# Kernel tuning notes

Hardware: AMD Instinct MI355X
Metric: run time of the kernel (lower is better)

Reference implementation:

```python
import jax, jax.numpy as jnp
import numpy as np

N, K = 4096, 256          # rays, samples per ray
V = 100000                # voxel table size
D = 64                    # field MLP hidden dim
SCALER = 7.0              # free-energy scaler from the source


def setup_inputs() -> dict:
    key = jax.random.key(0)
    ks = jax.random.split(key, 12)
    ray_start = jax.random.normal(ks[0], (N, 3), jnp.float32)
    rd = jax.random.normal(ks[1], (N, 3), jnp.float32)
    ray_dir = rd / jnp.linalg.norm(rd, axis=-1, keepdims=True)
    sampled_depth = jnp.sort(
        0.5 + 4.0 * jax.random.uniform(ks[2], (N, K), jnp.float32), axis=-1)
    sampled_dists = 0.02 * jax.random.uniform(ks[3], (N, K), jnp.float32)
    raw = jax.random.randint(ks[4], (N, K), 0, V + V // 4)
    sampled_idx = jnp.where(raw < V, raw, -1).astype(jnp.int64)
    voxel_color = 0.1 * jax.random.normal(ks[5], (V, 3), jnp.float32)
    W1 = jax.random.normal(ks[6], (6, D), jnp.float32) * (1.0 / np.sqrt(6.0))
    b1 = jnp.zeros((D,), jnp.float32)
    w_sigma = jax.random.normal(ks[7], (D, 1), jnp.float32) * (1.0 / np.sqrt(D))
    b_sigma = jnp.zeros((1,), jnp.float32)
    W_tex = jax.random.normal(ks[8], (D, 3), jnp.float32) * (1.0 / np.sqrt(D))
    b_tex = jnp.zeros((3,), jnp.float32)
    return dict(ray_start=ray_start, ray_dir=ray_dir,
                sampled_depth=sampled_depth, sampled_dists=sampled_dists,
                sampled_idx=sampled_idx, voxel_color=voxel_color,
                W1=W1, b1=b1, w_sigma=w_sigma, b_sigma=b_sigma,
                W_tex=W_tex, b_tex=b_tex)


def reference(ray_start, ray_dir, sampled_depth, sampled_dists, sampled_idx,
              voxel_color, W1, b1, w_sigma, b_sigma, W_tex, b_tex):
    mask = sampled_idx != -1                                   # [N,K] sample_mask
    # sampled_xyz = ray(start, dir, depth); sampled_dir broadcast of ray_dir
    xyz = ray_start[:, None, :] + ray_dir[:, None, :] * sampled_depth[..., None]
    dirs = jnp.broadcast_to(ray_dir[:, None, :], xyz.shape)    # [N,K,3]
    feat = jnp.concatenate([xyz, dirs], axis=-1)               # [N,K,6]
    # field_fn: small MLP -> sigma, texture
    h = jax.nn.relu(jnp.einsum('nkf,fd->nkd', feat, W1) + b1)  # [N,K,D]
    sigma = (jnp.einsum('nkd,do->nko', h, w_sigma) + b_sigma)[..., 0]  # [N,K]
    # voxel color embedding lookup (F.embedding); res=True adds it to texture
    idx_safe = jnp.where(mask, sampled_idx, 0)
    vcol = voxel_color[idx_safe]                               # [N,K,3] gather
    texture = jnp.einsum('nkd,dc->nkc', h, W_tex) + b_tex + vcol
    # free energy; masked_scatter == zero-out where mask is False
    free_energy = jnp.where(mask,
                            jax.nn.relu(sigma) * sampled_dists * SCALER, 0.0)
    texture = jnp.where(mask[..., None], texture, 0.0)
    # alpha compositing: a = 1-exp(-fe), b = exp(-cumsum(shifted fe))
    shifted = jnp.concatenate(
        [jnp.zeros((free_energy.shape[0], 1), free_energy.dtype),
         free_energy[:, :-1]], axis=-1)
    a = 1.0 - jnp.exp(-free_energy)
    b = jnp.exp(-jnp.cumsum(shifted, axis=-1))
    probs = a * b                                              # [N,K]
    depths = jnp.sum(sampled_depth * probs, axis=-1)           # [N]
    missed = 1.0 - jnp.sum(probs, axis=-1)                     # [N]
    colors = jnp.sum(texture * probs[..., None], axis=-2)      # [N,3]
    return colors, depths, missed, probs
```

## Files before the change

kernel.cpp:

```cpp
#include <hip/hip_runtime.h>

#define K_SAMP 256
#define D_HID 64
#define SCALER_FE 7.0f

typedef _Float16 half8  __attribute__((ext_vector_type(8)));
typedef __fp16   fp16x2 __attribute__((ext_vector_type(2)));
typedef float    f32x4  __attribute__((ext_vector_type(4)));

union H8U4 { half8 h; uint4 u; };
union H8P  { fp16x2 h2[4]; half8 h8; };

__device__ __forceinline__ half8 h8zero() {
    half8 a;
    #pragma unroll
    for (int j = 0; j < 8; ++j) a[j] = (_Float16)0.f;
    return a;
}

__global__ __launch_bounds__(256, 6)
void volrend_kernel(const float* __restrict__ ray_start,
                    const float* __restrict__ ray_dir,
                    const float* __restrict__ depth,
                    const float* __restrict__ dists,
                    const int*   __restrict__ vidx,
                    const float* __restrict__ vcol_tab,
                    const float* __restrict__ W1,
                    const float* __restrict__ b1,
                    const float* __restrict__ w_sigma,
                    const float* __restrict__ b_sigma,
                    const float* __restrict__ W_tex,
                    const float* __restrict__ b_tex,
                    float* __restrict__ out_colors,
                    float* __restrict__ out_depths,
                    float* __restrict__ out_missed,
                    float* __restrict__ out_probs) {
    __shared__ uint4 sFrag[6 * 64];
    __shared__ float sOut[K_SAMP][4];
    __shared__ float sTot[4];
    __shared__ float sRed[4][5];

    const int tid  = threadIdx.x;
    const int lane = tid & 63;
    const int wv   = tid >> 6;
    const int ray  = blockIdx.x;
    const int m    = lane & 15;
    const int g    = lane >> 4;

    if (tid < 64) {
        #pragma unroll
        for (int tt = 0; tt < 4; ++tt) {
            const int dim = 8 * (m >> 2) + (m & 3) + 4 * (tt & 1) + 32 * (tt >> 1);
            half8 a = h8zero();
            if (g == 0) {
                #pragma unroll
                for (int j = 0; j < 6; ++j) a[j] = (_Float16)W1[j * D_HID + dim];
                a[6] = (_Float16)b1[dim];
            }
            H8U4 c; c.h = a;
            sFrag[tt * 64 + lane] = c.u;
        }
        half8 a2a = h8zero(), a2b = h8zero();
        if (m < 4) {
            const int c = (m >= 1) ? (m - 1) : 0;
            #pragma unroll
            for (int j = 0; j < 8; ++j) {
                const int d = 8 * g + j;
                a2a[j] = (_Float16)((m == 0) ? w_sigma[d]      : W_tex[d * 3 + c]);
                a2b[j] = (_Float16)((m == 0) ? w_sigma[d + 32] : W_tex[(d + 32) * 3 + c]);
            }
        }
        H8U4 ca; ca.h = a2a; sFrag[4 * 64 + lane] = ca.u;
        H8U4 cb; cb.h = a2b; sFrag[5 * 64 + lane] = cb.u;
    }

    const float rs0 = ray_start[ray * 3 + 0];
    const float rs1 = ray_start[ray * 3 + 1];
    const float rs2 = ray_start[ray * 3 + 2];
    const float rd0 = ray_dir[ray * 3 + 0];
    const float rd1 = ray_dir[ray * 3 + 1];
    const float rd2 = ray_dir[ray * 3 + 2];
    const float bs  = b_sigma[0];
    const float bt0 = b_tex[0], bt1 = b_tex[1], bt2 = b_tex[2];

    __syncthreads();

    half8 a1[4];
    #pragma unroll
    for (int tt = 0; tt < 4; ++tt) { H8U4 c; c.u = sFrag[tt * 64 + lane]; a1[tt] = c.h; }
    H8U4 ca; ca.u = sFrag[4 * 64 + lane]; const half8 a2a = ca.h;
    H8U4 cb; cb.u = sFrag[5 * 64 + lane]; const half8 a2b = cb.h;

    f32x4 oinit = {0.f, 0.f, 0.f, 0.f};
    if (g == 0) { oinit[0] = bs; oinit[1] = bt0; oinit[2] = bt1; oinit[3] = bt2; }
    const f32x4 zero4 = {0.f, 0.f, 0.f, 0.f};

    const fp16x2 hc12 = __builtin_amdgcn_cvt_pkrtz(rd1, rd2);
    const fp16x2 hc3  = __builtin_amdgcn_cvt_pkrtz(1.0f, 0.0f);

    const size_t rayBase = (size_t)ray * K_SAMP;
    const int    qBase   = wv * 64;

    #pragma unroll
    for (int t = 0; t < 4; ++t) {
        const float dpt = depth[rayBase + qBase + 16 * t + m];
        const float fx = fmaf(rd0, dpt, rs0);
        const float fy = fmaf(rd1, dpt, rs1);
        const float fz = fmaf(rd2, dpt, rs2);
        H8P bb;
        bb.h2[0] = __builtin_amdgcn_cvt_pkrtz(fx, fy);
        bb.h2[1] = __builtin_amdgcn_cvt_pkrtz(fz, rd0);
        bb.h2[2] = hc12;
        bb.h2[3] = hc3;
        const f32x4 h0 = __builtin_amdgcn_mfma_f32_16x16x32_f16(a1[0], bb.h8, zero4, 0, 0, 0);
        const f32x4 h1 = __builtin_amdgcn_mfma_f32_16x16x32_f16(a1[1], bb.h8, zero4, 0, 0, 0);
        const f32x4 h2 = __builtin_amdgcn_mfma_f32_16x16x32_f16(a1[2], bb.h8, zero4, 0, 0, 0);
        const f32x4 h3 = __builtin_amdgcn_mfma_f32_16x16x32_f16(a1[3], bb.h8, zero4, 0, 0, 0);

        H8P p2a, p2b;
        p2a.h2[0] = __builtin_amdgcn_cvt_pkrtz(fmaxf(h0[0], 0.f), fmaxf(h0[1], 0.f));
        p2a.h2[1] = __builtin_amdgcn_cvt_pkrtz(fmaxf(h0[2], 0.f), fmaxf(h0[3], 0.f));
        p2a.h2[2] = __builtin_amdgcn_cvt_pkrtz(fmaxf(h1[0], 0.f), fmaxf(h1[1], 0.f));
        p2a.h2[3] = __builtin_amdgcn_cvt_pkrtz(fmaxf(h1[2], 0.f), fmaxf(h1[3], 0.f));
        p2b.h2[0] = __builtin_amdgcn_cvt_pkrtz(fmaxf(h2[0], 0.f), fmaxf(h2[1], 0.f));
        p2b.h2[1] = __builtin_amdgcn_cvt_pkrtz(fmaxf(h2[2], 0.f), fmaxf(h2[3], 0.f));
        p2b.h2[2] = __builtin_amdgcn_cvt_pkrtz(fmaxf(h3[0], 0.f), fmaxf(h3[1], 0.f));
        p2b.h2[3] = __builtin_amdgcn_cvt_pkrtz(fmaxf(h3[2], 0.f), fmaxf(h3[3], 0.f));

        f32x4 o = oinit;
        o = __builtin_amdgcn_mfma_f32_16x16x32_f16(a2a, p2a.h8, o, 0, 0, 0);
        o = __builtin_amdgcn_mfma_f32_16x16x32_f16(a2b, p2b.h8, o, 0, 0, 0);

        if (g == 0) {
            *(float4*)&sOut[qBase + 16 * t + m][0] = make_float4(o[0], o[1], o[2], o[3]);
        }
    }
    __syncthreads();

    const float dep = depth[rayBase + tid];
    const float dst = dists[rayBase + tid];
    const int   vi  = vidx[rayBase + tid];
    const bool  msk = (vi != -1);
    const int   vb  = (msk ? vi : 0) * 3;
    const float vc0 = vcol_tab[vb + 0];
    const float vc1 = vcol_tab[vb + 1];
    const float vc2 = vcol_tab[vb + 2];

    const float4 r4 = *(const float4*)&sOut[tid][0];
    float fe = 0.f, tA = 0.f, tB = 0.f, tC = 0.f;
    if (msk) {
        fe = fmaxf(r4.x, 0.f) * dst * SCALER_FE;
        tA = r4.y + vc0; tB = r4.z + vc1; tC = r4.w + vc2;
    }

    float x = fe;
    #pragma unroll
    for (int off = 1; off < 64; off <<= 1) {
        float v = __shfl_up(x, off, 64);
        if (lane >= off) x += v;
    }
    if (lane == 63) sTot[wv] = x;
    __syncthreads();
    float base = 0.f;
    #pragma unroll
    for (int w = 0; w < 3; ++w) {
        if (w < wv) base += sTot[w];
    }
    const float e0 = base + x - fe;
    const float p  = (1.0f - __expf(-fe)) * __expf(-e0);
    out_probs[rayBase + tid] = p;

    float sp = p;
    float sd = dep * p;
    float c0 = tA * p;
    float c1 = tB * p;
    float c2 = tC * p;
    #pragma unroll
    for (int off = 32; off > 0; off >>= 1) {
        sp += __shfl_down(sp, off, 64);
        sd += __shfl_down(sd, off, 64);
        c0 += __shfl_down(c0, off, 64);
        c1 += __shfl_down(c1, off, 64);
        c2 += __shfl_down(c2, off, 64);
    }
    if (lane == 0) {
        sRed[wv][0] = sp;
        sRed[wv][1] = sd;
        sRed[wv][2] = c0;
        sRed[wv][3] = c1;
        sRed[wv][4] = c2;
    }
    __syncthreads();
    if (tid < 5) {
        const float v = sRed[0][tid] + sRed[1][tid] + sRed[2][tid] + sRed[3][tid];
        if (tid == 0)      out_missed[ray] = 1.0f - v;
        else if (tid == 1) out_depths[ray] = v;
        else               out_colors[ray * 3 + (tid - 2)] = v;
    }
}

extern "C" void kernel_launch(void* const* d_in, const int* in_sizes, int n_in,
                              void* d_out, int out_size, void* d_ws, size_t ws_size,
                              hipStream_t stream) {
    const float* ray_start  = (const float*)d_in[0];
    const float* ray_dir    = (const float*)d_in[1];
    const float* depth      = (const float*)d_in[2];
    const float* dists      = (const float*)d_in[3];
    const int*   vidx       = (const int*)d_in[4];
    const float* vcol       = (const float*)d_in[5];
    const float* W1         = (const float*)d_in[6];
    const float* b1         = (const float*)d_in[7];
    const float* w_sigma    = (const float*)d_in[8];
    const float* b_sigma    = (const float*)d_in[9];
    const float* W_tex      = (const float*)d_in[10];
    const float* b_tex      = (const float*)d_in[11];

    const int N = in_sizes[0] / 3;
    float* out        = (float*)d_out;
    float* out_colors = out;
    float* out_depths = out + (size_t)N * 3;
    float* out_missed = out + (size_t)N * 3 + N;
    float* out_probs  = out + (size_t)N * 3 + 2 * (size_t)N;

    volrend_kernel<<<N, 256, 0, stream>>>(
        ray_start, ray_dir, depth, dists, vidx, vcol,
        W1, b1, w_sigma, b_sigma, W_tex, b_tex,
        out_colors, out_depths, out_missed, out_probs);
}
```

Before: 21.05 us.

## Map one ray per wavefront with DPP scans and vectorized per-lane samples

Each wavefront now handles a whole ray (four rays per block), processing 16 MFMA tiles per wave. Each lane owns four consecutive samples loaded as float4. The cross-wave scan and reductions, with their shared-memory handoffs and block barriers, become DPP-based inclusive scans within the wave. Gathers and loads are issued before the MFMA loop so their latency can overlap with compute. In exchange, shared memory per block grows to four ray buffers, and the occupancy hint drops from 6 to 4 blocks.

```diff
diff --git a/kernel.cpp b/kernel.cpp
--- a/kernel.cpp
+++ b/kernel.cpp
@@ -18,7 +18,21 @@
     return a;
 }
 
-__global__ __launch_bounds__(256, 6)
+#define DPP_ADD(x, ctrl, rowmask)                                              \
+    (x) += __int_as_float(__builtin_amdgcn_update_dpp(                         \
+        0, __float_as_int(x), (ctrl), (rowmask), 0xf, false))
+
+__device__ __forceinline__ float dpp_scan_incl(float x) {
+    DPP_ADD(x, 0x111, 0xf);
+    DPP_ADD(x, 0x112, 0xf);
+    DPP_ADD(x, 0x114, 0xf);
+    DPP_ADD(x, 0x118, 0xf);
+    DPP_ADD(x, 0x142, 0xa);
+    DPP_ADD(x, 0x143, 0xc);
+    return x;
+}
+
+__global__ __launch_bounds__(256, 4)
 void volrend_kernel(const float* __restrict__ ray_start,
                     const float* __restrict__ ray_dir,
                     const float* __restrict__ depth,
@@ -36,14 +50,12 @@
                     float* __restrict__ out_missed,
                     float* __restrict__ out_probs) {
     __shared__ uint4 sFrag[6 * 64];
-    __shared__ float sOut[K_SAMP][4];
-    __shared__ float sTot[4];
-    __shared__ float sRed[4][5];
+    __shared__ float sOut[4][K_SAMP][4];
 
     const int tid  = threadIdx.x;
     const int lane = tid & 63;
     const int wv   = tid >> 6;
-    const int ray  = blockIdx.x;
+    const int ray  = __builtin_amdgcn_readfirstlane(blockIdx.x * 4 + wv);
     const int m    = lane & 15;
     const int g    = lane >> 4;
 
@@ -83,6 +95,22 @@
     const float bs  = b_sigma[0];
     const float bt0 = b_tex[0], bt1 = b_tex[1], bt2 = b_tex[2];
 
+    const size_t rayBase = (size_t)ray * K_SAMP;
+    const float4 dep4 = ((const float4*)(depth + rayBase))[lane];
+    const float4 dst4 = ((const float4*)(dists + rayBase))[lane];
+    const int4   vi4  = ((const int4*)(vidx  + rayBase))[lane];
+    const int via[4] = {vi4.x, vi4.y, vi4.z, vi4.w};
+    bool  msk[4];
+    float vc[4][3];
+    #pragma unroll
+    for (int s = 0; s < 4; ++s) {
+        msk[s] = (via[s] != -1);
+        const int b = (msk[s] ? via[s] : 0) * 3;
+        vc[s][0] = vcol_tab[b + 0];
+        vc[s][1] = vcol_tab[b + 1];
+        vc[s][2] = vcol_tab[b + 2];
+    }
+
     __syncthreads();
 
     half8 a1[4];
@@ -98,12 +126,9 @@
     const fp16x2 hc12 = __builtin_amdgcn_cvt_pkrtz(rd1, rd2);
     const fp16x2 hc3  = __builtin_amdgcn_cvt_pkrtz(1.0f, 0.0f);
 
-    const size_t rayBase = (size_t)ray * K_SAMP;
-    const int    qBase   = wv * 64;
-
-    #pragma unroll
-    for (int t = 0; t < 4; ++t) {
-        const float dpt = depth[rayBase + qBase + 16 * t + m];
+    #pragma unroll 4
+    for (int t = 0; t < 16; ++t) {
+        const float dpt = depth[rayBase + 16 * t + m];
         const float fx = fmaf(rd0, dpt, rs0);
         const float fy = fmaf(rd1, dpt, rs1);
         const float fz = fmaf(rd2, dpt, rs2);
@@ -132,70 +157,51 @@
         o = __builtin_amdgcn_mfma_f32_16x16x32_f16(a2b, p2b.h8, o, 0, 0, 0);
 
         if (g == 0) {
-            *(float4*)&sOut[qBase + 16 * t + m][0] = make_float4(o[0], o[1], o[2], o[3]);
-        }
-    }
-    __syncthreads();
-
-    const float dep = depth[rayBase + tid];
-    const float dst = dists[rayBase + tid];
-    const int   vi  = vidx[rayBase + tid];
-    const bool  msk = (vi != -1);
-    const int   vb  = (msk ? vi : 0) * 3;
-    const float vc0 = vcol_tab[vb + 0];
-    const float vc1 = vcol_tab[vb + 1];
-    const float vc2 = vcol_tab[vb + 2];
-
-    const float4 r4 = *(const float4*)&sOut[tid][0];
-    float fe = 0.f, tA = 0.f, tB = 0.f, tC = 0.f;
-    if (msk) {
-        fe = fmaxf(r4.x, 0.f) * dst * SCALER_FE;
-        tA = r4.y + vc0; tB = r4.z + vc1; tC = r4.w + vc2;
-    }
-
-    float x = fe;
-    #pragma unroll
-    for (int off = 1; off < 64; off <<= 1) {
-        float v = __shfl_up(x, off, 64);
-        if (lane >= off) x += v;
-    }
-    if (lane == 63) sTot[wv] = x;
-    __syncthreads();
-    float base = 0.f;
-    #pragma unroll
-    for (int w = 0; w < 3; ++w) {
-        if (w < wv) base += sTot[w];
-    }
-    const float e0 = base + x - fe;
-    const float p  = (1.0f - __expf(-fe)) * __expf(-e0);
-    out_probs[rayBase + tid] = p;
-
-    float sp = p;
-    float sd = dep * p;
-    float c0 = tA * p;
-    float c1 = tB * p;
-    float c2 = tC * p;
-    #pragma unroll
-    for (int off = 32; off > 0; off >>= 1) {
-        sp += __shfl_down(sp, off, 64);
-        sd += __shfl_down(sd, off, 64);
-        c0 += __shfl_down(c0, off, 64);
-        c1 += __shfl_down(c1, off, 64);
-        c2 += __shfl_down(c2, off, 64);
-    }
-    if (lane == 0) {
-        sRed[wv][0] = sp;
-        sRed[wv][1] = sd;
-        sRed[wv][2] = c0;
-        sRed[wv][3] = c1;
-        sRed[wv][4] = c2;
-    }
-    __syncthreads();
-    if (tid < 5) {
-        const float v = sRed[0][tid] + sRed[1][tid] + sRed[2][tid] + sRed[3][tid];
-        if (tid == 0)      out_missed[ray] = 1.0f - v;
-        else if (tid == 1) out_depths[ray] = v;
-        else               out_colors[ray * 3 + (tid - 2)] = v;
+            *(float4*)&sOut[wv][16 * t + m][0] = make_float4(o[0], o[1], o[2], o[3]);
+        }
+    }
+
+    const float depa[4] = {dep4.x, dep4.y, dep4.z, dep4.w};
+    const float dsta[4] = {dst4.x, dst4.y, dst4.z, dst4.w};
+    float fe[4], tA[4], tB[4], tC[4];
+    #pragma unroll
+    for (int s = 0; s < 4; ++s) {
+        const float4 r4 = *(const float4*)&sOut[wv][4 * lane + s][0];
+        if (msk[s]) {
+            fe[s] = fmaxf(r4.x, 0.f) * dsta[s] * SCALER_FE;
+            tA[s] = r4.y + vc[s][0];
+            tB[s] = r4.z + vc[s][1];
+            tC[s] = r4.w + vc[s][2];
+        } else {
+            fe[s] = 0.f; tA[s] = 0.f; tB[s] = 0.f; tC[s] = 0.f;
+        }
+    }
+
+    const float T = fe[0] + fe[1] + fe[2] + fe[3];
+    const float x = dpp_scan_incl(T);
+    const float e0 = x - T;
+    const float e1 = e0 + fe[0];
+    const float e2 = e1 + fe[1];
+    const float e3 = e2 + fe[2];
+
+    const float p0 = (1.0f - __expf(-fe[0])) * __expf(-e0);
+    const float p1 = (1.0f - __expf(-fe[1])) * __expf(-e1);
+    const float p2 = (1.0f - __expf(-fe[2])) * __expf(-e2);
+    const float p3 = (1.0f - __expf(-fe[3])) * __expf(-e3);
+
+    ((float4*)(out_probs + rayBase))[lane] = make_float4(p0, p1, p2, p3);
+
+    float sp = dpp_scan_incl(p0 + p1 + p2 + p3);
+    float sd = dpp_scan_incl(depa[0] * p0 + depa[1] * p1 + depa[2] * p2 + depa[3] * p3);
+    float c0 = dpp_scan_incl(tA[0] * p0 + tA[1] * p1 + tA[2] * p2 + tA[3] * p3);
+    float c1 = dpp_scan_incl(tB[0] * p0 + tB[1] * p1 + tB[2] * p2 + tB[3] * p3);
+    float c2 = dpp_scan_incl(tC[0] * p0 + tC[1] * p1 + tC[2] * p2 + tC[3] * p3);
+    if (lane == 63) {
+        out_colors[ray * 3 + 0] = c0;
+        out_colors[ray * 3 + 1] = c1;
+        out_colors[ray * 3 + 2] = c2;
+        out_depths[ray] = sd;
+        out_missed[ray] = 1.0f - sp;
     }
 }
 
@@ -222,7 +228,7 @@
     float* out_missed = out + (size_t)N * 3 + N;
     float* out_probs  = out + (size_t)N * 3 + 2 * (size_t)N;
 
-    volrend_kernel<<<N, 256, 0, stream>>>(
+    volrend_kernel<<<N / 4, 256, 0, stream>>>(
         ray_start, ray_dir, depth, dists, vidx, vcol,
         W1, b1, w_sigma, b_sigma, W_tex, b_tex,
         out_colors, out_depths, out_missed, out_probs);
```

New measurement: 19.39 us. -7.9%, faster.
